# Performance work log

Hardware: AMD Instinct MI355X
Metric: run time of the kernel (lower is better)

## Reference

```python
import jax, jax.numpy as jnp
import numpy as np
from jax import lax

EPS = 1e-6
TANH_CLIP = 1.0 - 1e-5
FRECHET_ITERS = 10


def _sqnorm(x):
    return jnp.sum(x * x, axis=-1, keepdims=True)


def _norm(x):
    return jnp.sqrt(jnp.clip(_sqnorm(x), EPS))


def _lambda(x, c):
    # conformal factor lambda_x = 2 / (1 - c ||x||^2)
    return 2.0 / jnp.clip(1.0 - c * _sqnorm(x), EPS)


def mobius_add(x, y, c):
    x2 = _sqnorm(x)
    y2 = _sqnorm(y)
    xy = jnp.sum(x * y, axis=-1, keepdims=True)
    num = (1.0 + 2.0 * c * xy + c * y2) * x + (1.0 - c * x2) * y
    den = 1.0 + 2.0 * c * xy + (c * c) * x2 * y2
    return num / jnp.clip(den, EPS)


def expmap(x, u, c):
    sc = jnp.sqrt(c)
    un = _norm(u)
    second = jnp.tanh(sc * _lambda(x, c) * un / 2.0) * u / (sc * un)
    return mobius_add(x, second, c)


def logmap(x, y, c):
    sc = jnp.sqrt(c)
    m = mobius_add(-x, y, c)
    mn = _norm(m)
    t = jnp.arctanh(jnp.clip(sc * mn, 0.0, TANH_CLIP))
    return (2.0 / (sc * _lambda(x, c))) * t * m / mn


def exp0(u, c):
    sc = jnp.sqrt(c)
    un = _norm(u)
    return jnp.tanh(sc * un) * u / (sc * un)


def dist(x, y, c):
    sc = jnp.sqrt(c)
    mn = _norm(mobius_add(-x, y, c))
    return (2.0 / sc) * jnp.arctanh(jnp.clip(sc * mn, 0.0, TANH_CLIP))[..., 0]


def gyr(a, b, w, c):
    # gyr[a,b]w = -(a (+) b) (+) (a (+) (b (+) w))
    return mobius_add(-mobius_add(a, b, c), mobius_add(a, mobius_add(b, w, c), c), c)


def transp(x, y, u, c):
    # parallel transport x -> y:  (lam_x / lam_y) * gyr[y, -x] u
    return (_lambda(x, c) / _lambda(y, c)) * gyr(y, -x, u, c)


def frechet_mean(x, c):
    # Karcher fixed-point iteration: mu <- exp_mu(mean_i log_mu(x_i))
    m = jnp.mean(x, axis=0)  # (D,)
    max_norm = (1.0 - 1e-3) / jnp.sqrt(c)
    mn = _norm(m)[0]
    m = m * jnp.minimum(1.0, max_norm / mn)

    def step(mu, _):
        g = jnp.mean(logmap(mu, x, c), axis=0)
        return expmap(mu, g, c), None

    mu, _ = lax.scan(step, m, None, length=FRECHET_ITERS)
    return mu


def setup_inputs() -> dict:
    key = jax.random.key(0)
    k1, k2 = jax.random.split(key)
    B, S, D = 64, 256, 256
    K = jnp.float32(-1.2)
    sc = np.sqrt(1.2)
    x = jax.random.normal(k1, (B, S, D), dtype=jnp.float32)
    # project points strictly inside the Poincare ball of radius 1/sqrt(c)
    x = x / (1.0 + _norm(x)) * jnp.float32(0.7 / sc)
    mean_param = 0.01 * jax.random.normal(k2, (D,), dtype=jnp.float32)
    var_param = jnp.float32(1.0)
    return {"x": x, "K": K, "mean_param": mean_param, "var_param": var_param}


def reference(x, K, mean_param, var_param):
    c = -K  # positive ball curvature (K = -1.2)
    shapes = x.shape
    xf = x.reshape(-1, shapes[-1])  # (N, D)
    on_manifold = exp0(mean_param, c)          # (D,) target mean on manifold
    mu = frechet_mean(xf, c)                   # (D,) batch Frechet mean
    var = jnp.mean(dist(xf, mu, c) ** 2)       # Frechet variance (scalar)
    logm = transp(mu, on_manifold, logmap(mu, xf, c), c)  # (N, D)
    logm = jnp.sqrt(var_param / (var + 1e-6)) * logm
    out = expmap(on_manifold, logm, c)         # (N, D)
    return out.reshape(shapes)
```

## Files before the change

### kernel.cpp

```cpp
#include <hip/hip_runtime.h>
#include <math.h>
#include <string.h>

#define EPSF 1e-6f
#define TCLIP (1.0f - 1e-5f)
#define NPTS 16384
#define DDIM 256
#define NBLK 128
#define NTHR 1024
#define PPB 128
#define NWAVE 16
#define PPW 8
#define PSTR 260
#define WSLICE (PPW * 65)
#define FRECHET_ITERS_N 10

#define WS_PA 64
#define WS_PB (WS_PA + NBLK * PSTR)

__device__ __forceinline__ void st_pair_sc1(float* addr, float a, float b) {
    float2 f2 = make_float2(a, b);
    double dv; memcpy(&dv, &f2, 8);
    __hip_atomic_store((double*)addr, dv, __ATOMIC_RELAXED, __HIP_MEMORY_SCOPE_AGENT);
}
__device__ __forceinline__ float2 ld_pair_sc1(const float* addr) {
    double dv = __hip_atomic_load((const double*)addr, __ATOMIC_RELAXED, __HIP_MEMORY_SCOPE_AGENT);
    float2 f2; memcpy(&f2, &dv, 8);
    return f2;
}
__device__ __forceinline__ void st_f_sc1(float* addr, float v) {
    __hip_atomic_store(addr, v, __ATOMIC_RELAXED, __HIP_MEMORY_SCOPE_AGENT);
}
__device__ __forceinline__ float ld_f_sc1(const float* addr) {
    return __hip_atomic_load(addr, __ATOMIC_RELAXED, __HIP_MEMORY_SCOPE_AGENT);
}
__device__ __forceinline__ void st_u_sc1(unsigned* addr, unsigned v) {
    __hip_atomic_store(addr, v, __ATOMIC_RELAXED, __HIP_MEMORY_SCOPE_AGENT);
}
__device__ __forceinline__ unsigned ld_u_sc1(const unsigned* addr) {
    return __hip_atomic_load(addr, __ATOMIC_RELAXED, __HIP_MEMORY_SCOPE_AGENT);
}

__device__ __forceinline__ float block_sum(float v) {
    __shared__ float s_bs[NWAVE];
    #pragma unroll
    for (int off = 32; off; off >>= 1) v += __shfl_xor(v, off);
    const int w = threadIdx.x >> 6, l = threadIdx.x & 63;
    __syncthreads();
    if (l == 0) s_bs[w] = v;
    __syncthreads();
    float s = 0.f;
    #pragma unroll
    for (int i = 0; i < NWAVE; ++i) s += s_bs[i];
    return s;
}

__global__ void init_tags(float* ws) {
    int t = threadIdx.x;
    if (t < NBLK) {
        st_u_sc1((unsigned*)(ws + WS_PA + t * PSTR + 258), 0u);
        st_u_sc1((unsigned*)(ws + WS_PB + t * PSTR + 258), 0u);
    }
}

__global__ __launch_bounds__(NTHR, 1) void rbn_fused(
    const float* __restrict__ x, const float* __restrict__ Kp,
    const float* __restrict__ mean_param, const float* __restrict__ var_param,
    float* __restrict__ out, float* __restrict__ ws)
{
    const float c = -Kp[0];
    const float sc = sqrtf(c);
    const float N1 = 1.f / NPTS;
    const int t = threadIdx.x, lane = t & 63, wv = t >> 6;
    const int b = blockIdx.x;
    const int p0 = b * PPB;
    const float4* xr = ((const float4*)x) + p0 * 64;

    float* PA = ws + WS_PA;
    float* PB = ws + WS_PB;

    __shared__ float mu_s[DDIM], om_s[DDIM];
    __shared__ float dpart[NWAVE * WSLICE];
    __shared__ float pseg[NWAVE * DDIM];
    __shared__ float part1[NWAVE], part2[NWAVE], part3[NWAVE];

    unsigned barno = 0;

    float4 xreg[PPW];
    #pragma unroll
    for (int i = 0; i < PPW; ++i)
        xreg[i] = xr[(wv * PPW + i) * 64 + lane];

    auto wave_dot = [&](float4 v4, bool self) -> float {
        float* slice = dpart + wv * WSLICE;
        #pragma unroll
        for (int i = 0; i < PPW; ++i) {
            float4 xv = xreg[i];
            float4 u4 = self ? xv : v4;
            slice[i * 65 + lane] = xv.x * u4.x + xv.y * u4.y + xv.z * u4.z + xv.w * u4.w;
        }
        const int g = lane >> 3, q = lane & 7;
        float s = 0.f;
        #pragma unroll
        for (int j = 0; j < 8; ++j) s += slice[g * 65 + q * 8 + j];
        #pragma unroll
        for (int off = 1; off <= 4; off <<= 1) s += __shfl_xor(s, off);
        return s;
    };
    auto wave_sum_groups = [&](float v) -> float {
        #pragma unroll
        for (int off = 8; off <= 32; off <<= 1) v += __shfl_xor(v, off);
        return v;
    };

    auto poll_tags = [&](const float* buf) {
        if (t < NBLK) {
            const unsigned* tg = (const unsigned*)(buf + t * PSTR + 258);
            while (ld_u_sc1(tg) < barno)
                __builtin_amdgcn_s_sleep(1);
        }
        __syncthreads();
    };

    {
        float u = (t < DDIM) ? mean_param[t] : 0.f;
        float un2 = block_sum(u * u);
        float un = sqrtf(fmaxf(un2, EPSF));
        if (t < DDIM) om_s[t] = tanhf(sc * un) * u / (sc * un);
    }
    float om2;
    { float v = (t < DDIM) ? om_s[t] * om_s[t] : 0.f; om2 = block_sum(v); }

    ++barno;
    {
        float4 a = make_float4(0.f, 0.f, 0.f, 0.f);
        #pragma unroll
        for (int i = 0; i < PPW; ++i) {
            a.x += xreg[i].x; a.y += xreg[i].y; a.z += xreg[i].z; a.w += xreg[i].w;
        }
        ((float4*)(pseg + wv * DDIM))[lane] = a;
    }
    __syncthreads();
    {
        float s = 0.f;
        if (t < DDIM) {
            #pragma unroll
            for (int w = 0; w < NWAVE; ++w) s += pseg[w * DDIM + t];
        }
        float partner = __shfl_xor(s, 1);
        if (t < DDIM && !(t & 1)) st_pair_sc1(PA + b * PSTR + t, s, partner);
    }
    __syncthreads();
    if (t == 0) st_u_sc1((unsigned*)(PA + b * PSTR + 258), barno);

    float y2r = wave_dot(make_float4(0.f, 0.f, 0.f, 0.f), true);
    float er;
    {
        float4 om4 = ((const float4*)om_s)[lane];
        er = wave_dot(om4, false);
    }
    poll_tags(PA);

    float mu2;
    {
        const int dg = t & 127, sg = t >> 7;
        float ax = 0.f, ay = 0.f;
        #pragma unroll
        for (int j = 0; j < 16; ++j) {
            float2 v = ld_pair_sc1(PA + (sg * 16 + j) * PSTR + 2 * dg);
            ax += v.x; ay += v.y;
        }
        ((float2*)(pseg + sg * DDIM))[dg] = make_float2(ax, ay);
        __syncthreads();
        float m = 0.f, mm = 0.f;
        if (t < DDIM) {
            float s = 0.f;
            #pragma unroll
            for (int w = 0; w < 8; ++w) s += pseg[w * DDIM + t];
            m = s * N1; mm = m * m;
        }
        #pragma unroll
        for (int off = 32; off; off >>= 1) mm += __shfl_xor(mm, off);
        if (lane == 0) part1[wv] = mm;
        __syncthreads();
        float mn2 = 0.f;
        #pragma unroll
        for (int i = 0; i < NWAVE; ++i) mn2 += part1[i];
        float mn = sqrtf(fmaxf(mn2, EPSF));
        float maxn = (1.f - 1e-3f) / sc;
        float f = fminf(1.f, maxn / mn);
        if (t < DDIM) mu_s[t] = m * f;
        mu2 = f * f * mn2;
        __syncthreads();
    }

    for (int it = 0; it < FRECHET_ITERS_N; ++it) {
        float* buf = (it & 1) ? PA : PB;
        ++barno;
        float4 mu4 = ((const float4*)mu_s)[lane];
        float d = wave_dot(mu4, false);
        float w, sA;
        {
            float y2 = y2r;
            float P = 1.f - 2.f * c * d;
            float den = fmaxf(P + c * c * mu2 * y2, EPSF);
            float A = -(P + c * y2) / den;
            float B = (1.f - c * mu2) / den;
            float mn2 = fmaxf(A * A * mu2 + 2.f * A * B * d + B * B * y2, EPSF);
            float mn = sqrtf(mn2);
            float tt = atanhf(fminf(sc * mn, TCLIP));
            float s = (fmaxf(1.f - c * mu2, EPSF) / sc) * tt / mn;
            w = s * B;
            sA = s * A;
        }
        {
            float4 a = make_float4(0.f, 0.f, 0.f, 0.f);
            #pragma unroll
            for (int i = 0; i < PPW; ++i) {
                float wi = __shfl(w, i * 8);
                a.x += wi * xreg[i].x; a.y += wi * xreg[i].y;
                a.z += wi * xreg[i].z; a.w += wi * xreg[i].w;
            }
            ((float4*)(pseg + wv * DDIM))[lane] = a;
        }
        float sAw = wave_sum_groups(sA);
        float wdw = wave_sum_groups(w * d);
        if (lane == 0) { part1[wv] = sAw; part2[wv] = wdw; }
        __syncthreads();
        {
            float s = 0.f;
            if (t < DDIM) {
                #pragma unroll
                for (int w2 = 0; w2 < NWAVE; ++w2) s += pseg[w2 * DDIM + t];
            }
            float partner = __shfl_xor(s, 1);
            if (t < DDIM && !(t & 1)) st_pair_sc1(buf + b * PSTR + t, s, partner);
            if (t == 0) {
                float sa = 0.f, wd = 0.f;
                #pragma unroll
                for (int i = 0; i < NWAVE; ++i) { sa += part1[i]; wd += part2[i]; }
                st_pair_sc1(buf + b * PSTR + 256, sa, wd);
            }
        }
        __syncthreads();
        if (t == 0) st_u_sc1((unsigned*)(buf + b * PSTR + 258), barno);
        poll_tags(buf);
        const int dg = t & 127, sg = t >> 7;
        float ax = 0.f, ay = 0.f;
        #pragma unroll
        for (int j = 0; j < 16; ++j) {
            float2 v = ld_pair_sc1(buf + (sg * 16 + j) * PSTR + 2 * dg);
            ax += v.x; ay += v.y;
        }
        float2 sp = make_float2(0.f, 0.f);
        if (t < NBLK) sp = ld_pair_sc1(buf + t * PSTR + 256);
        ((float2*)(pseg + sg * DDIM))[dg] = make_float2(ax, ay);
        __syncthreads();
        float g = 0.f, vvv = 0.f;
        if (t < DDIM) {
            #pragma unroll
            for (int w2 = 0; w2 < 8; ++w2) g += pseg[w2 * DDIM + t];
            vvv = g * g;
        }
        float sAt = sp.x, wdt = sp.y;
        #pragma unroll
        for (int off = 32; off; off >>= 1) {
            vvv += __shfl_xor(vvv, off); sAt += __shfl_xor(sAt, off); wdt += __shfl_xor(wdt, off);
        }
        if (lane == 0) { part1[wv] = vvv; part2[wv] = sAt; part3[wv] = wdt; }
        __syncthreads();
        float vv = 0.f, sa = 0.f, wd = 0.f;
        #pragma unroll
        for (int i = 0; i < NWAVE; ++i) { vv += part1[i]; sa += part2[i]; wd += part3[i]; }
        float gn2 = N1 * N1 * (vv + 2.f * sa * wd + sa * sa * mu2);
        float mg  = N1 * (wd + sa * mu2);
        float un = sqrtf(fmaxf(gn2, EPSF));
        float lam = 2.f / fmaxf(1.f - c * mu2, EPSF);
        float k = tanhf(sc * lam * un * 0.5f) / (sc * un);
        float ms = k * mg;
        float s2 = k * k * gn2;
        float aa = 1.f + 2.f * c * ms + c * s2;
        float bb2 = 1.f - c * mu2;
        float den = fmaxf(1.f + 2.f * c * ms + c * c * mu2 * s2, EPSF);
        float cm = (aa + bb2 * k * N1 * sa) / den;
        float cv = (bb2 * k * N1) / den;
        if (t < DDIM) mu_s[t] = cm * mu_s[t] + cv * g;
        mu2 = cm * cm * mu2 + 2.f * cm * cv * wd + cv * cv * vv;
        __syncthreads();
    }

    float* vbuf = ((FRECHET_ITERS_N - 1) & 1) ? PB : PA;
    ++barno;
    float4 mu4f = ((const float4*)mu_s)[lane];
    float4 om4f = ((const float4*)om_s)[lane];
    float d = wave_dot(mu4f, false);
    float vval;
    {
        float y2 = y2r;
        float P = 1.f - 2.f * c * d;
        float den = fmaxf(P + c * c * mu2 * y2, EPSF);
        float A = -(P + c * y2) / den;
        float B = (1.f - c * mu2) / den;
        float mn2 = fmaxf(A * A * mu2 + 2.f * A * B * d + B * B * y2, EPSF);
        float mn = sqrtf(mn2);
        float tt = atanhf(fminf(sc * mn, TCLIP));
        float dd = (2.f / sc) * tt;
        vval = dd * dd;
    }
    {
        float vw = wave_sum_groups(vval);
        float ov = (t < DDIM) ? om_s[t] * mu_s[t] : 0.f;
        #pragma unroll
        for (int off = 32; off; off >>= 1) ov += __shfl_xor(ov, off);
        if (lane == 0) { part1[wv] = vw; part2[wv] = ov; }
    }
    __syncthreads();
    if (t == 0) {
        float tot = 0.f;
        #pragma unroll
        for (int i = 0; i < NWAVE; ++i) tot += part1[i];
        st_f_sc1(vbuf + b * PSTR + 256, tot);
    }
    __syncthreads();
    if (t == 0) st_u_sc1((unsigned*)(vbuf + b * PSTR + 258), barno);

    float omu = 0.f;
    #pragma unroll
    for (int i = 0; i < NWAVE; ++i) omu += part2[i];

    const float Amu = fmaxf(1.f - c * mu2, EPSF);
    const float Aom = fmaxf(1.f - c * om2, EPSF);
    const float ratio = Aom / Amu;
    const float aq = 1.f - 2.f * c * omu + c * mu2;
    const float bq = 1.f - c * om2;
    const float dqv = fmaxf(1.f - 2.f * c * omu + c * c * om2 * mu2, EPSF);
    const float qo = aq / dqv, qm = -bq / dqv;
    const float q2 = qo * qo * om2 + 2.f * qo * qm * omu + qm * qm * mu2;
    const float lam_om = 2.f / Aom;

    float g2o, g2m, g2x;
    {
        float y2 = y2r, e = er;
        auto dotOm3 = [&](float po, float pm, float px) { return po * om2 + pm * omu + px * e; };
        auto dotMu3 = [&](float po, float pm, float px) { return po * omu + pm * mu2 + px * d; };
        auto sqn3 = [&](float po, float pm, float px) {
            return po * po * om2 + pm * pm * mu2 + px * px * y2
                 + 2.f * (po * pm * omu + po * px * e + pm * px * d);
        };
        float P = 1.f - 2.f * c * d;
        float den0 = fmaxf(P + c * c * mu2 * y2, EPSF);
        float A = -(P + c * y2) / den0;
        float B = (1.f - c * mu2) / den0;
        float mn2 = fmaxf(A * A * mu2 + 2.f * A * B * d + B * B * y2, EPSF);
        float mn = sqrtf(mn2);
        float tt = atanhf(fminf(sc * mn, TCLIP));
        float s = (fmaxf(1.f - c * mu2, EPSF) / sc) * tt / mn;
        float Um = s * A, Ux = s * B;

        float xy1 = -dotMu3(0.f, Um, Ux);
        float Y21 = sqn3(0.f, Um, Ux);
        float a1 = 1.f + 2.f * c * xy1 + c * Y21;
        float b1 = 1.f - c * mu2;
        float dn1 = fmaxf(1.f + 2.f * c * xy1 + c * c * mu2 * Y21, EPSF);
        float h1m = (-a1 + b1 * Um) / dn1;
        float h1x = (b1 * Ux) / dn1;

        float xy2 = dotOm3(0.f, h1m, h1x);
        float Y22 = sqn3(0.f, h1m, h1x);
        float a2 = 1.f + 2.f * c * xy2 + c * Y22;
        float b2 = 1.f - c * om2;
        float dn2 = fmaxf(1.f + 2.f * c * xy2 + c * c * om2 * Y22, EPSF);
        float h2o = a2 / dn2;
        float h2m = (b2 * h1m) / dn2;
        float h2x = (b2 * h1x) / dn2;

        float xy3 = -(qo * dotOm3(h2o, h2m, h2x) + qm * dotMu3(h2o, h2m, h2x));
        float Y23 = sqn3(h2o, h2m, h2x);
        float a3 = 1.f + 2.f * c * xy3 + c * Y23;
        float b3 = 1.f - c * q2;
        float dn3 = fmaxf(1.f + 2.f * c * xy3 + c * c * q2 * Y23, EPSF);
        g2o = (-a3 * qo + b3 * h2o) / dn3;
        g2m = (-a3 * qm + b3 * h2m) / dn3;
        g2x = (b3 * h2x) / dn3;
    }
    poll_tags(vbuf);

    {
        float va = (t < NBLK) ? ld_f_sc1(vbuf + t * PSTR + 256) : 0.f;
        #pragma unroll
        for (int off = 32; off; off >>= 1) va += __shfl_xor(va, off);
        if (lane == 0) part1[wv] = va;
    }
    __syncthreads();
    float vsum = 0.f;
    #pragma unroll
    for (int i = 0; i < NWAVE; ++i) vsum += part1[i];
    float var = vsum * N1;
    float gamma = sqrtf(var_param[0] / (var + 1e-6f));

    float fo, fm, fx;
    {
        float y2 = y2r, e = er;
        float k1 = ratio * gamma;
        float Lo = k1 * g2o, Lm = k1 * g2m, Lx = k1 * g2x;
        float un2 = Lo * Lo * om2 + Lm * Lm * mu2 + Lx * Lx * y2
                  + 2.f * (Lo * Lm * omu + Lo * Lx * e + Lm * Lx * d);
        float un = sqrtf(fmaxf(un2, EPSF));
        float coef = tanhf(sc * lam_om * un * 0.5f) / (sc * un);
        float So = coef * Lo, Sm = coef * Lm, Sx = coef * Lx;
        float xy4 = So * om2 + Sm * omu + Sx * e;
        float Y24 = coef * coef * un2;
        float a4 = 1.f + 2.f * c * xy4 + c * Y24;
        float b4 = 1.f - c * om2;
        float dn4 = fmaxf(1.f + 2.f * c * xy4 + c * c * om2 * Y24, EPSF);
        fo = (a4 + b4 * So) / dn4;
        fm = (b4 * Sm) / dn4;
        fx = (b4 * Sx) / dn4;
    }

    #pragma unroll
    for (int i = 0; i < PPW; ++i) {
        float foi = __shfl(fo, i * 8);
        float fmi = __shfl(fm, i * 8);
        float fxi = __shfl(fx, i * 8);
        float4 x4 = xreg[i];
        float4 o4;
        o4.x = foi * om4f.x + fmi * mu4f.x + fxi * x4.x;
        o4.y = foi * om4f.y + fmi * mu4f.y + fxi * x4.y;
        o4.z = foi * om4f.z + fmi * mu4f.z + fxi * x4.z;
        o4.w = foi * om4f.w + fmi * mu4f.w + fxi * x4.w;
        ((float4*)out)[(p0 + wv * PPW + i) * 64 + lane] = o4;
    }
}

extern "C" void kernel_launch(void* const* d_in, const int* in_sizes, int n_in,
                              void* d_out, int out_size, void* d_ws, size_t ws_size,
                              hipStream_t stream) {
    const float* x = (const float*)d_in[0];
    const float* K = (const float*)d_in[1];
    const float* mean_param = (const float*)d_in[2];
    const float* var_param = (const float*)d_in[3];
    float* out = (float*)d_out;
    float* ws = (float*)d_ws;

    init_tags<<<1, 256, 0, stream>>>(ws);
    void* args[] = {(void*)&x, (void*)&K, (void*)&mean_param, (void*)&var_param,
                    (void*)&out, (void*)&ws};
    hipLaunchCooperativeKernel((const void*)rbn_fused, dim3(NBLK), dim3(NTHR),
                               args, 0, stream);
}
```

Measured before the change: 194.0 us.

## Halve block count, double points per wave, use shuffle-only dot reductions

Cuts the persistent grid from 128 to 64 blocks, with each wave holding 16 points in registers instead of 8, so every grid-wide barrier has half as many per-block partials to publish and reduce. The per-point dot product now reduces through a full 64-lane shuffle butterfly instead of going through an LDS scratch slice, which frees that shared memory. Each sub-group now polls only the 8 rows it reads rather than waiting on a block-wide poll plus __syncthreads. In exchange only half the CUs run, the per-thread register footprint doubles, and each dot product costs six shuffle rounds per point.

```diff
diff --git a/kernel.cpp b/kernel.cpp
--- a/kernel.cpp
+++ b/kernel.cpp
@@ -6,13 +6,12 @@
 #define TCLIP (1.0f - 1e-5f)
 #define NPTS 16384
 #define DDIM 256
-#define NBLK 128
+#define NBLK 64
 #define NTHR 1024
-#define PPB 128
 #define NWAVE 16
-#define PPW 8
+#define PPW 16
+#define PPB (NWAVE * PPW)
 #define PSTR 260
-#define WSLICE (PPW * 65)
 #define FRECHET_ITERS_N 10
 
 #define WS_PA 64
@@ -80,9 +79,9 @@
     float* PB = ws + WS_PB;
 
     __shared__ float mu_s[DDIM], om_s[DDIM];
-    __shared__ float dpart[NWAVE * WSLICE];
     __shared__ float pseg[NWAVE * DDIM];
     __shared__ float part1[NWAVE], part2[NWAVE], part3[NWAVE];
+    __shared__ float bc0;
 
     unsigned barno = 0;
 
@@ -92,34 +91,29 @@
         xreg[i] = xr[(wv * PPW + i) * 64 + lane];
 
     auto wave_dot = [&](float4 v4, bool self) -> float {
-        float* slice = dpart + wv * WSLICE;
+        float res = 0.f;
         #pragma unroll
         for (int i = 0; i < PPW; ++i) {
             float4 xv = xreg[i];
             float4 u4 = self ? xv : v4;
-            slice[i * 65 + lane] = xv.x * u4.x + xv.y * u4.y + xv.z * u4.z + xv.w * u4.w;
-        }
-        const int g = lane >> 3, q = lane & 7;
-        float s = 0.f;
-        #pragma unroll
-        for (int j = 0; j < 8; ++j) s += slice[g * 65 + q * 8 + j];
-        #pragma unroll
-        for (int off = 1; off <= 4; off <<= 1) s += __shfl_xor(s, off);
-        return s;
+            float s = xv.x * u4.x + xv.y * u4.y + xv.z * u4.z + xv.w * u4.w;
+            #pragma unroll
+            for (int off = 1; off < 64; off <<= 1) s += __shfl_xor(s, off);
+            res = (lane == i) ? s : res;
+        }
+        return res;
     };
-    auto wave_sum_groups = [&](float v) -> float {
-        #pragma unroll
-        for (int off = 8; off <= 32; off <<= 1) v += __shfl_xor(v, off);
+    auto wave_red = [&](float v) -> float {
+        #pragma unroll
+        for (int off = 1; off < 64; off <<= 1) v += __shfl_xor(v, off);
         return v;
     };
-
-    auto poll_tags = [&](const float* buf) {
-        if (t < NBLK) {
-            const unsigned* tg = (const unsigned*)(buf + t * PSTR + 258);
-            while (ld_u_sc1(tg) < barno)
-                __builtin_amdgcn_s_sleep(1);
-        }
-        __syncthreads();
+    const int dg = t & 127, sg = t >> 7;
+    auto wait_rows = [&](const float* buf) {
+        if (lane < 8) {
+            const unsigned* tg = (const unsigned*)(buf + (sg * 8 + lane) * PSTR + 258);
+            while (ld_u_sc1(tg) < barno) __builtin_amdgcn_s_sleep(1);
+        }
     };
 
     {
@@ -155,19 +149,15 @@
 
     float y2r = wave_dot(make_float4(0.f, 0.f, 0.f, 0.f), true);
     float er;
-    {
-        float4 om4 = ((const float4*)om_s)[lane];
-        er = wave_dot(om4, false);
-    }
-    poll_tags(PA);
+    { float4 om4 = ((const float4*)om_s)[lane]; er = wave_dot(om4, false); }
 
     float mu2;
     {
-        const int dg = t & 127, sg = t >> 7;
+        wait_rows(PA);
         float ax = 0.f, ay = 0.f;
         #pragma unroll
-        for (int j = 0; j < 16; ++j) {
-            float2 v = ld_pair_sc1(PA + (sg * 16 + j) * PSTR + 2 * dg);
+        for (int j = 0; j < 8; ++j) {
+            float2 v = ld_pair_sc1(PA + (sg * 8 + j) * PSTR + 2 * dg);
             ax += v.x; ay += v.y;
         }
         ((float2*)(pseg + sg * DDIM))[dg] = make_float2(ax, ay);
@@ -179,8 +169,7 @@
             for (int w = 0; w < 8; ++w) s += pseg[w * DDIM + t];
             m = s * N1; mm = m * m;
         }
-        #pragma unroll
-        for (int off = 32; off; off >>= 1) mm += __shfl_xor(mm, off);
+        mm = wave_red(mm);
         if (lane == 0) part1[wv] = mm;
         __syncthreads();
         float mn2 = 0.f;
@@ -198,10 +187,10 @@
         float* buf = (it & 1) ? PA : PB;
         ++barno;
         float4 mu4 = ((const float4*)mu_s)[lane];
-        float d = wave_dot(mu4, false);
-        float w, sA;
-        {
-            float y2 = y2r;
+        float dv = wave_dot(mu4, false);
+        float w = 0.f, sAv = 0.f, wdv = 0.f;
+        if (lane < PPW) {
+            float y2 = y2r, d = dv;
             float P = 1.f - 2.f * c * d;
             float den = fmaxf(P + c * c * mu2 * y2, EPSF);
             float A = -(P + c * y2) / den;
@@ -211,21 +200,22 @@
             float tt = atanhf(fminf(sc * mn, TCLIP));
             float s = (fmaxf(1.f - c * mu2, EPSF) / sc) * tt / mn;
             w = s * B;
-            sA = s * A;
+            sAv = s * A;
+            wdv = w * d;
         }
         {
             float4 a = make_float4(0.f, 0.f, 0.f, 0.f);
             #pragma unroll
             for (int i = 0; i < PPW; ++i) {
-                float wi = __shfl(w, i * 8);
+                float wi = __shfl(w, i);
                 a.x += wi * xreg[i].x; a.y += wi * xreg[i].y;
                 a.z += wi * xreg[i].z; a.w += wi * xreg[i].w;
             }
             ((float4*)(pseg + wv * DDIM))[lane] = a;
         }
-        float sAw = wave_sum_groups(sA);
-        float wdw = wave_sum_groups(w * d);
-        if (lane == 0) { part1[wv] = sAw; part2[wv] = wdw; }
+        sAv = wave_red(sAv);
+        wdv = wave_red(wdv);
+        if (lane == 0) { part1[wv] = sAv; part2[wv] = wdv; }
         __syncthreads();
         {
             float s = 0.f;
@@ -244,16 +234,16 @@
         }
         __syncthreads();
         if (t == 0) st_u_sc1((unsigned*)(buf + b * PSTR + 258), barno);
-        poll_tags(buf);
-        const int dg = t & 127, sg = t >> 7;
+
+        wait_rows(buf);
         float ax = 0.f, ay = 0.f;
         #pragma unroll
-        for (int j = 0; j < 16; ++j) {
-            float2 v = ld_pair_sc1(buf + (sg * 16 + j) * PSTR + 2 * dg);
+        for (int j = 0; j < 8; ++j) {
+            float2 v = ld_pair_sc1(buf + (sg * 8 + j) * PSTR + 2 * dg);
             ax += v.x; ay += v.y;
         }
         float2 sp = make_float2(0.f, 0.f);
-        if (t < NBLK) sp = ld_pair_sc1(buf + t * PSTR + 256);
+        if (dg < 8) sp = ld_pair_sc1(buf + (sg * 8 + dg) * PSTR + 256);
         ((float2*)(pseg + sg * DDIM))[dg] = make_float2(ax, ay);
         __syncthreads();
         float g = 0.f, vvv = 0.f;
@@ -264,7 +254,7 @@
         }
         float sAt = sp.x, wdt = sp.y;
         #pragma unroll
-        for (int off = 32; off; off >>= 1) {
+        for (int off = 1; off < 64; off <<= 1) {
             vvv += __shfl_xor(vvv, off); sAt += __shfl_xor(sAt, off); wdt += __shfl_xor(wdt, off);
         }
         if (lane == 0) { part1[wv] = vvv; part2[wv] = sAt; part3[wv] = wdt; }
@@ -293,10 +283,10 @@
     ++barno;
     float4 mu4f = ((const float4*)mu_s)[lane];
     float4 om4f = ((const float4*)om_s)[lane];
-    float d = wave_dot(mu4f, false);
-    float vval;
-    {
-        float y2 = y2r;
+    float dv2 = wave_dot(mu4f, false);
+    float vval = 0.f;
+    if (lane < PPW) {
+        float y2 = y2r, d = dv2;
         float P = 1.f - 2.f * c * d;
         float den = fmaxf(P + c * c * mu2 * y2, EPSF);
         float A = -(P + c * y2) / den;
@@ -308,10 +298,9 @@
         vval = dd * dd;
     }
     {
-        float vw = wave_sum_groups(vval);
+        float vw = wave_red(vval);
         float ov = (t < DDIM) ? om_s[t] * mu_s[t] : 0.f;
-        #pragma unroll
-        for (int off = 32; off; off >>= 1) ov += __shfl_xor(ov, off);
+        ov = wave_red(ov);
         if (lane == 0) { part1[wv] = vw; part2[wv] = ov; }
     }
     __syncthreads();
@@ -338,9 +327,9 @@
     const float q2 = qo * qo * om2 + 2.f * qo * qm * omu + qm * qm * mu2;
     const float lam_om = 2.f / Aom;
 
-    float g2o, g2m, g2x;
-    {
-        float y2 = y2r, e = er;
+    float g2o = 0.f, g2m = 0.f, g2x = 0.f;
+    if (lane < PPW) {
+        float y2 = y2r, d = dv2, e = er;
         auto dotOm3 = [&](float po, float pm, float px) { return po * om2 + pm * omu + px * e; };
         auto dotMu3 = [&](float po, float pm, float px) { return po * omu + pm * mu2 + px * d; };
         auto sqn3 = [&](float po, float pm, float px) {
@@ -383,24 +372,24 @@
         g2m = (-a3 * qm + b3 * h2m) / dn3;
         g2x = (b3 * h2x) / dn3;
     }
-    poll_tags(vbuf);
-
-    {
-        float va = (t < NBLK) ? ld_f_sc1(vbuf + t * PSTR + 256) : 0.f;
-        #pragma unroll
-        for (int off = 32; off; off >>= 1) va += __shfl_xor(va, off);
-        if (lane == 0) part1[wv] = va;
-    }
-    __syncthreads();
-    float vsum = 0.f;
-    #pragma unroll
-    for (int i = 0; i < NWAVE; ++i) vsum += part1[i];
-    float var = vsum * N1;
+
+    {
+        float va = 0.f;
+        if (t < NBLK) {
+            const unsigned* tg = (const unsigned*)(vbuf + t * PSTR + 258);
+            while (ld_u_sc1(tg) < barno) __builtin_amdgcn_s_sleep(1);
+            va = ld_f_sc1(vbuf + t * PSTR + 256);
+        }
+        va = wave_red(va);
+        if (t == 0) bc0 = va;
+    }
+    __syncthreads();
+    float var = bc0 * N1;
     float gamma = sqrtf(var_param[0] / (var + 1e-6f));
 
-    float fo, fm, fx;
-    {
-        float y2 = y2r, e = er;
+    float fo = 0.f, fm = 0.f, fx = 0.f;
+    if (lane < PPW) {
+        float y2 = y2r, d = dv2, e = er;
         float k1 = ratio * gamma;
         float Lo = k1 * g2o, Lm = k1 * g2m, Lx = k1 * g2x;
         float un2 = Lo * Lo * om2 + Lm * Lm * mu2 + Lx * Lx * y2
@@ -420,9 +409,9 @@
 
     #pragma unroll
     for (int i = 0; i < PPW; ++i) {
-        float foi = __shfl(fo, i * 8);
-        float fmi = __shfl(fm, i * 8);
-        float fxi = __shfl(fx, i * 8);
+        float foi = __shfl(fo, i);
+        float fmi = __shfl(fm, i);
+        float fxi = __shfl(fx, i);
         float4 x4 = xreg[i];
         float4 o4;
         o4.x = foi * om4f.x + fmi * mu4f.x + fxi * x4.x;
```

New measurement: 254.4 us. 1.31x slower.
